# Optimization experiments

Measured on AMD Instinct MI355X. Metric: run time of the kernel, lower is better.

The kernel has to match this reference:

```python
import jax, jax.numpy as jnp
import numpy as np

NUM_HEADS = 16
EMB = 1024
HEAD_DIM = EMB // NUM_HEADS


def setup_inputs() -> dict:
    key = jax.random.key(0)
    ks = jax.random.split(key, 9)
    N, L = 2, 2048
    return {
        "keys": jax.random.normal(ks[0], (N, L, EMB), dtype=jnp.float32),
        "queries": jax.random.normal(ks[1], (N, L, EMB), dtype=jnp.float32),
        "values": jax.random.normal(ks[2], (N, L, EMB), dtype=jnp.float32),
        "mask": jax.random.randint(ks[3], (N, L), 0, 2, dtype=jnp.int32),
        "Wk": jax.random.normal(ks[4], (HEAD_DIM, HEAD_DIM), dtype=jnp.float32) * 0.05,
        "Wq": jax.random.normal(ks[5], (HEAD_DIM, HEAD_DIM), dtype=jnp.float32) * 0.05,
        "Wv": jax.random.normal(ks[6], (HEAD_DIM, HEAD_DIM), dtype=jnp.float32) * 0.05,
        "Wo": jax.random.normal(ks[7], (EMB, EMB), dtype=jnp.float32) * 0.02,
        "bo": jax.random.normal(ks[8], (EMB,), dtype=jnp.float32) * 0.02,
    }


def reference(keys, queries, values, mask, Wk, Wq, Wv, Wo, bo):
    N, Q, E = queries.shape
    H, D = NUM_HEADS, HEAD_DIM
    # reshape to heads: [N, L, H, D]
    k = keys.reshape(N, -1, H, D) @ Wk.T
    q = queries.reshape(N, -1, H, D) @ Wq.T
    # faithful to source bug: values are the v-projection of the projected queries
    v = q @ Wv.T
    # energy: [N, H, Q, K]
    energy = jnp.einsum("nqhd,nkhd->nhqk", q, k)
    m = mask[:, None, None, :]  # [N,1,1,K]
    energy = jnp.where(m == 0, jnp.float32(-1e20), energy)
    p = jax.nn.softmax(energy / jnp.sqrt(jnp.float32(E)), axis=3)
    attn = jnp.einsum("nhqk,nkhd->nqhd", p, v).reshape(N, Q, E)
    return attn @ Wo.T + bo
```

## Files before the change

### kernel.cpp

```cpp
#include <hip/hip_runtime.h>
#include <cmath>

constexpr int N_ = 2;
constexpr int L_ = 2048;
constexpr int H_ = 16;
constexpr int E_ = 1024;
constexpr int ROWS_ = N_ * L_ * H_;

typedef __attribute__((ext_vector_type(8))) short bf16x8;
typedef __attribute__((ext_vector_type(4))) float f32x4;
typedef unsigned short ushort_t;
#define MFMA16(a, b, c) __builtin_amdgcn_mfma_f32_16x16x32_bf16(a, b, c, 0, 0, 0)

__device__ __forceinline__ unsigned short f2bf(float x) {
    union { float f; unsigned u; } v; v.f = x;
    return (unsigned short)((v.u + 0x7fffu + ((v.u >> 16) & 1u)) >> 16);
}
__device__ __forceinline__ unsigned pack2(float a, float b) {
    return (unsigned)f2bf(a) | ((unsigned)f2bf(b) << 16);
}

__global__ __launch_bounds__(256) void proj_kernel(
    const float* __restrict__ keys, const float* __restrict__ queries,
    const float* __restrict__ Wk, const float* __restrict__ Wq, const float* __restrict__ Wv,
    ushort_t* __restrict__ qo, ushort_t* __restrict__ ko, ushort_t* __restrict__ vto)
{
    constexpr int P = 72;
    __shared__ __align__(16) ushort_t Xq[64 * P];
    __shared__ __align__(16) ushort_t Xk[64 * P];
    __shared__ __align__(16) ushort_t Wqs[64 * P];
    __shared__ __align__(16) ushort_t Wks[64 * P];
    __shared__ __align__(16) ushort_t Wvs[64 * P];
    const int tid = threadIdx.x;
    const int lt = blockIdx.x & 31;
    const int h  = (blockIdx.x >> 5) & 15;
    const int n  = blockIdx.x >> 9;
    const int r0 = tid >> 4, c4 = (tid & 15) * 4;

#pragma unroll
    for (int j = 0; j < 4; ++j) {
        const int r = r0 + 16 * j;
        const size_t xoff = (size_t)(n * L_ + lt * 64 + r) * E_ + h * 64 + c4;
        const float4 xq = *(const float4*)&queries[xoff];
        const float4 xk = *(const float4*)&keys[xoff];
        const float4 wq = *(const float4*)&Wq[r * 64 + c4];
        const float4 wk = *(const float4*)&Wk[r * 64 + c4];
        const float4 wv = *(const float4*)&Wv[r * 64 + c4];
        *(uint2*)&Xq[r * P + c4]  = make_uint2(pack2(xq.x, xq.y), pack2(xq.z, xq.w));
        *(uint2*)&Xk[r * P + c4]  = make_uint2(pack2(xk.x, xk.y), pack2(xk.z, xk.w));
        *(uint2*)&Wqs[r * P + c4] = make_uint2(pack2(wq.x, wq.y), pack2(wq.z, wq.w));
        *(uint2*)&Wks[r * P + c4] = make_uint2(pack2(wk.x, wk.y), pack2(wk.z, wk.w));
        *(uint2*)&Wvs[r * P + c4] = make_uint2(pack2(wv.x, wv.y), pack2(wv.z, wv.w));
    }
    __syncthreads();

    const int wave = tid >> 6, lane = tid & 63;
    const int quad = lane >> 4, l16 = lane & 15;
    const int arow = (wave * 16 + l16) * P;
    const f32x4 zero = (f32x4){0.f, 0.f, 0.f, 0.f};

    bf16x8 a0 = *(const bf16x8*)&Xq[arow + quad * 8];
    bf16x8 a1 = *(const bf16x8*)&Xq[arow + 32 + quad * 8];
    bf16x8 c0 = *(const bf16x8*)&Xk[arow + quad * 8];
    bf16x8 c1 = *(const bf16x8*)&Xk[arow + 32 + quad * 8];
    f32x4 qf[4], kf[4];
#pragma unroll
    for (int nt = 0; nt < 4; ++nt) {
        const int brow = (nt * 16 + l16) * P;
        f32x4 acc = MFMA16(a0, *(const bf16x8*)&Wqs[brow + quad * 8], zero);
        qf[nt] = MFMA16(a1, *(const bf16x8*)&Wqs[brow + 32 + quad * 8], acc);
        acc = MFMA16(c0, *(const bf16x8*)&Wks[brow + quad * 8], zero);
        kf[nt] = MFMA16(c1, *(const bf16x8*)&Wks[brow + 32 + quad * 8], acc);
    }
    __syncthreads();

    const int crow = wave * 16 + quad * 4;
#pragma unroll
    for (int nt = 0; nt < 4; ++nt)
#pragma unroll
        for (int reg = 0; reg < 4; ++reg) {
            Xq[(crow + reg) * P + nt * 16 + l16]  = f2bf(qf[nt][reg]);
            Wqs[(crow + reg) * P + nt * 16 + l16] = f2bf(kf[nt][reg]);
        }
    asm volatile("s_waitcnt lgkmcnt(0)" ::: "memory");

    bf16x8 va0 = *(const bf16x8*)&Xq[arow + quad * 8];
    bf16x8 va1 = *(const bf16x8*)&Xq[arow + 32 + quad * 8];
    f32x4 vf[4];
#pragma unroll
    for (int nt = 0; nt < 4; ++nt) {
        const int brow = (nt * 16 + l16) * P;
        f32x4 acc = MFMA16(va0, *(const bf16x8*)&Wvs[brow + quad * 8], zero);
        vf[nt] = MFMA16(va1, *(const bf16x8*)&Wvs[brow + 32 + quad * 8], acc);
    }
#pragma unroll
    for (int nt = 0; nt < 4; ++nt)
#pragma unroll
        for (int reg = 0; reg < 4; ++reg)
            Xk[(nt * 16 + l16) * P + crow + reg] = f2bf(vf[nt][reg]);
    __syncthreads();

#pragma unroll
    for (int j = 0; j < 4; ++j) {
        const int r = r0 + 16 * j;
        const size_t qkoff = (size_t)(n * L_ + lt * 64 + r) * E_ + h * 64 + c4;
        *(uint2*)&qo[qkoff] = *(const uint2*)&Xq[r * P + c4];
        *(uint2*)&ko[qkoff] = *(const uint2*)&Wqs[r * P + c4];
        const size_t vtoff = ((size_t)(n * H_ + h) * 64 + r) * L_ + lt * 64 + c4;
        *(uint2*)&vto[vtoff] = *(const uint2*)&Xk[r * P + c4];
    }
}

__global__ __launch_bounds__(256) void attn_kernel(
    const ushort_t* __restrict__ q, const ushort_t* __restrict__ k,
    const ushort_t* __restrict__ vt, const int* __restrict__ mask,
    ushort_t* __restrict__ attn)
{
    constexpr int P = 72;
    constexpr float CEXP = 0.04508422002778010648f;
    __shared__ __align__(16) ushort_t Qs[64 * P];
    __shared__ __align__(16) ushort_t Ks[64 * P];
    __shared__ __align__(16) ushort_t VTs[64 * P];
    __shared__ __align__(16) ushort_t Ps[64 * P];
    __shared__ float Msk[64];

    const int tid = threadIdx.x;
    const int qt = blockIdx.x & 31;
    const int h  = (blockIdx.x >> 5) & 15;
    const int n  = blockIdx.x >> 9;
    const int r0 = tid >> 4, c4 = (tid & 15) * 4;

#pragma unroll
    for (int j = 0; j < 4; ++j) {
        const int r = r0 + 16 * j;
        *(uint2*)&Qs[r * P + c4] =
            *(const uint2*)&q[(size_t)(n * L_ + qt * 64 + r) * E_ + h * 64 + c4];
    }
    const size_t kbase = (size_t)n * L_ * E_ + h * 64 + c4;
    const size_t vbase = (size_t)(n * H_ + h) * 64 * L_ + c4;
    uint2 kr[4], vr[4];
#pragma unroll
    for (int j = 0; j < 4; ++j) {
        const int r = r0 + 16 * j;
        kr[j] = *(const uint2*)&k[kbase + (size_t)r * E_];
        vr[j] = *(const uint2*)&vt[vbase + (size_t)r * L_];
    }
    int mr = (tid < 64) ? mask[n * L_ + tid] : 0;
    __syncthreads();

    const int wave = tid >> 6, lane = tid & 63;
    const int quad = lane >> 4, l16 = lane & 15;
    const f32x4 zero = (f32x4){0.f, 0.f, 0.f, 0.f};
    const bf16x8 aq0 = *(const bf16x8*)&Qs[(wave * 16 + l16) * P + quad * 8];
    const bf16x8 aq1 = *(const bf16x8*)&Qs[(wave * 16 + l16) * P + 32 + quad * 8];

    float lrow[4] = {0.f, 0.f, 0.f, 0.f};
    f32x4 O[4];
#pragma unroll
    for (int r = 0; r < 4; ++r) O[r] = zero;

    for (int t = 0; t < 32; ++t) {
#pragma unroll
        for (int j = 0; j < 4; ++j) {
            const int r = r0 + 16 * j;
            *(uint2*)&Ks[r * P + c4]  = kr[j];
            *(uint2*)&VTs[r * P + c4] = vr[j];
        }
        if (tid < 64) Msk[tid] = mr ? 0.f : -1e9f;
        __syncthreads();

        const int tt = (t < 31) ? t + 1 : 31;
#pragma unroll
        for (int j = 0; j < 4; ++j) {
            const int r = r0 + 16 * j;
            kr[j] = *(const uint2*)&k[kbase + (size_t)(tt * 64 + r) * E_];
            vr[j] = *(const uint2*)&vt[vbase + (size_t)r * L_ + tt * 64];
        }
        if (tid < 64) mr = mask[n * L_ + tt * 64 + tid];

        f32x4 s[4];
#pragma unroll
        for (int nk = 0; nk < 4; ++nk) {
            const int brow = (nk * 16 + l16) * P;
            f32x4 acc = MFMA16(aq0, *(const bf16x8*)&Ks[brow + quad * 8], zero);
            s[nk] = MFMA16(aq1, *(const bf16x8*)&Ks[brow + 32 + quad * 8], acc);
        }
        float mc[4];
#pragma unroll
        for (int nk = 0; nk < 4; ++nk) mc[nk] = Msk[nk * 16 + l16];

#pragma unroll
        for (int reg = 0; reg < 4; ++reg) {
            const int prow = (wave * 16 + quad * 4 + reg) * P;
            float ls = 0.f;
#pragma unroll
            for (int nk = 0; nk < 4; ++nk) {
                const float e = __builtin_amdgcn_exp2f(fmaf(s[nk][reg], CEXP, mc[nk]));
                ls += e;
                Ps[prow + nk * 16 + l16] = f2bf(e);
            }
            lrow[reg] += ls;
        }
        asm volatile("s_waitcnt lgkmcnt(0)" ::: "memory");

        const bf16x8 ap0 = *(const bf16x8*)&Ps[(wave * 16 + l16) * P + quad * 8];
        const bf16x8 ap1 = *(const bf16x8*)&Ps[(wave * 16 + l16) * P + 32 + quad * 8];
#pragma unroll
        for (int dt = 0; dt < 4; ++dt) {
            const int brow = (dt * 16 + l16) * P;
            O[dt] = MFMA16(ap0, *(const bf16x8*)&VTs[brow + quad * 8], O[dt]);
            O[dt] = MFMA16(ap1, *(const bf16x8*)&VTs[brow + 32 + quad * 8], O[dt]);
        }
        __syncthreads();
    }

#pragma unroll
    for (int reg = 0; reg < 4; ++reg) {
        float s = lrow[reg];
        s += __shfl_xor(s, 1); s += __shfl_xor(s, 2);
        s += __shfl_xor(s, 4); s += __shfl_xor(s, 8);
        lrow[reg] = 1.f / s;
    }
#pragma unroll
    for (int dt = 0; dt < 4; ++dt)
#pragma unroll
        for (int reg = 0; reg < 4; ++reg) {
            const size_t rowg = (size_t)(n * L_ + qt * 64 + wave * 16 + quad * 4 + reg);
            attn[rowg * E_ + h * 64 + dt * 16 + l16] = f2bf(O[dt][reg] * lrow[reg]);
        }
}

__global__ __launch_bounds__(256) void conv_wo_kernel(
    const float* __restrict__ Wo, ushort_t* __restrict__ Wob)
{
    const int i = (blockIdx.x * 256 + threadIdx.x) * 4;
    const float4 w = *(const float4*)&Wo[i];
    *(uint2*)&Wob[i] = make_uint2(pack2(w.x, w.y), pack2(w.z, w.w));
}

__global__ __launch_bounds__(256) void outproj_kernel(
    const ushort_t* __restrict__ attn, const ushort_t* __restrict__ Wob,
    const float* __restrict__ bo, float* __restrict__ out)
{
    constexpr int P = 72;
    __shared__ __align__(16) ushort_t As[64 * P];
    __shared__ __align__(16) ushort_t Bs[128 * P];
    const int tid = threadIdx.x;
    const int bc = (blockIdx.x & 7) * 128;
    const int br = (blockIdx.x >> 3) * 64;
    const int r0 = tid >> 4, c4 = (tid & 15) * 4;
    const int wave = tid >> 6, lane = tid & 63;
    const int quad = lane >> 4, l16 = lane & 15;

    uint2 ar[4], brg[8];
#pragma unroll
    for (int j = 0; j < 4; ++j)
        ar[j] = *(const uint2*)&attn[(size_t)(br + r0 + 16 * j) * E_ + c4];
#pragma unroll
    for (int j = 0; j < 8; ++j)
        brg[j] = *(const uint2*)&Wob[(size_t)(bc + r0 + 16 * j) * E_ + c4];

    f32x4 acc[8];
#pragma unroll
    for (int nt = 0; nt < 8; ++nt) acc[nt] = (f32x4){0.f, 0.f, 0.f, 0.f};

    for (int kt = 0; kt < 16; ++kt) {
#pragma unroll
        for (int j = 0; j < 4; ++j) *(uint2*)&As[(r0 + 16 * j) * P + c4] = ar[j];
#pragma unroll
        for (int j = 0; j < 8; ++j) *(uint2*)&Bs[(r0 + 16 * j) * P + c4] = brg[j];
        __syncthreads();
        const int knext = (kt < 15) ? (kt + 1) * 64 : kt * 64;
#pragma unroll
        for (int j = 0; j < 4; ++j)
            ar[j] = *(const uint2*)&attn[(size_t)(br + r0 + 16 * j) * E_ + knext + c4];
#pragma unroll
        for (int j = 0; j < 8; ++j)
            brg[j] = *(const uint2*)&Wob[(size_t)(bc + r0 + 16 * j) * E_ + knext + c4];

        const bf16x8 a0 = *(const bf16x8*)&As[(wave * 16 + l16) * P + quad * 8];
        const bf16x8 a1 = *(const bf16x8*)&As[(wave * 16 + l16) * P + 32 + quad * 8];
#pragma unroll
        for (int nt = 0; nt < 8; ++nt) {
            const int brow = (nt * 16 + l16) * P;
            acc[nt] = MFMA16(a0, *(const bf16x8*)&Bs[brow + quad * 8], acc[nt]);
            acc[nt] = MFMA16(a1, *(const bf16x8*)&Bs[brow + 32 + quad * 8], acc[nt]);
        }
        __syncthreads();
    }
#pragma unroll
    for (int nt = 0; nt < 8; ++nt) {
        const float b = bo[bc + nt * 16 + l16];
#pragma unroll
        for (int reg = 0; reg < 4; ++reg)
            out[(size_t)(br + wave * 16 + quad * 4 + reg) * E_ + bc + nt * 16 + l16] =
                acc[nt][reg] + b;
    }
}

extern "C" void kernel_launch(void* const* d_in, const int* in_sizes, int n_in,
                              void* d_out, int out_size, void* d_ws, size_t ws_size,
                              hipStream_t stream)
{
    const float* keys    = (const float*)d_in[0];
    const float* queries = (const float*)d_in[1];
    const int*   mask    = (const int*)d_in[3];
    const float* Wk      = (const float*)d_in[4];
    const float* Wq      = (const float*)d_in[5];
    const float* Wv      = (const float*)d_in[6];
    const float* Wo      = (const float*)d_in[7];
    const float* bo      = (const float*)d_in[8];
    float* out = (float*)d_out;

    ushort_t* qbf  = (ushort_t*)d_ws;
    ushort_t* kbf  = qbf + (size_t)ROWS_ * 64;
    ushort_t* vtbf = kbf + (size_t)ROWS_ * 64;
    ushort_t* abf  = vtbf + (size_t)ROWS_ * 64;
    ushort_t* wob  = abf + (size_t)ROWS_ * 64;

    conv_wo_kernel<<<E_ * E_ / 1024, 256, 0, stream>>>(Wo, wob);
    proj_kernel<<<N_ * H_ * (L_ / 64), 256, 0, stream>>>(keys, queries, Wk, Wq, Wv,
                                                         qbf, kbf, vtbf);
    attn_kernel<<<N_ * H_ * (L_ / 64), 256, 0, stream>>>(qbf, kbf, vtbf, mask, abf);
    outproj_kernel<<<(N_ * L_ / 64) * (E_ / 128), 256, 0, stream>>>(abf, wob, bo, out);
}
```

Baseline: 206.7 us.

## Restructure attention into single-wave blocks with register-resident K/V and transposed S

```diff
diff --git a/kernel.cpp b/kernel.cpp
--- a/kernel.cpp
+++ b/kernel.cpp
@@ -111,131 +111,146 @@
     }
 }
 
-__global__ __launch_bounds__(256) void attn_kernel(
+__global__ __launch_bounds__(64, 2) void attn_kernel(
     const ushort_t* __restrict__ q, const ushort_t* __restrict__ k,
-    const ushort_t* __restrict__ vt, const int* __restrict__ mask,
+    const ushort_t* __restrict__ vt, const float* __restrict__ maskf,
     ushort_t* __restrict__ attn)
 {
     constexpr int P = 72;
     constexpr float CEXP = 0.04508422002778010648f;
-    __shared__ __align__(16) ushort_t Qs[64 * P];
-    __shared__ __align__(16) ushort_t Ks[64 * P];
-    __shared__ __align__(16) ushort_t VTs[64 * P];
-    __shared__ __align__(16) ushort_t Ps[64 * P];
-    __shared__ float Msk[64];
-
-    const int tid = threadIdx.x;
-    const int qt = blockIdx.x & 31;
-    const int h  = (blockIdx.x >> 5) & 15;
-    const int n  = blockIdx.x >> 9;
-    const int r0 = tid >> 4, c4 = (tid & 15) * 4;
-
-#pragma unroll
-    for (int j = 0; j < 4; ++j) {
-        const int r = r0 + 16 * j;
-        *(uint2*)&Qs[r * P + c4] =
-            *(const uint2*)&q[(size_t)(n * L_ + qt * 64 + r) * E_ + h * 64 + c4];
-    }
-    const size_t kbase = (size_t)n * L_ * E_ + h * 64 + c4;
-    const size_t vbase = (size_t)(n * H_ + h) * 64 * L_ + c4;
-    uint2 kr[4], vr[4];
-#pragma unroll
-    for (int j = 0; j < 4; ++j) {
-        const int r = r0 + 16 * j;
-        kr[j] = *(const uint2*)&k[kbase + (size_t)r * E_];
-        vr[j] = *(const uint2*)&vt[vbase + (size_t)r * L_];
-    }
-    int mr = (tid < 64) ? mask[n * L_ + tid] : 0;
-    __syncthreads();
-
-    const int wave = tid >> 6, lane = tid & 63;
-    const int quad = lane >> 4, l16 = lane & 15;
-    const f32x4 zero = (f32x4){0.f, 0.f, 0.f, 0.f};
-    const bf16x8 aq0 = *(const bf16x8*)&Qs[(wave * 16 + l16) * P + quad * 8];
-    const bf16x8 aq1 = *(const bf16x8*)&Qs[(wave * 16 + l16) * P + 32 + quad * 8];
-
-    float lrow[4] = {0.f, 0.f, 0.f, 0.f};
-    f32x4 O[4];
-#pragma unroll
-    for (int r = 0; r < 4; ++r) O[r] = zero;
+    __shared__ __align__(16) ushort_t Ps[32 * P];
+    __shared__ __align__(16) float Ls[32];
+
+    const int b = blockIdx.x;
+    const int qt = b & 63;
+    const int h  = (b >> 6) & 15;
+    const int n  = b >> 10;
+    const int lane = threadIdx.x;
+    const int l16 = lane & 15, quad = lane >> 4;
+
+    const ushort_t* kh = k  + (size_t)n * L_ * E_ + h * 64;
+    const ushort_t* vh = vt + (size_t)(n * H_ + h) * 64 * L_;
+    const float*    mh = maskf + n * L_;
+    const size_t qrow0 = (size_t)(n * L_ + qt * 32);
+
+    bf16x8 qb[2][2];
+#pragma unroll
+    for (int s = 0; s < 2; ++s)
+#pragma unroll
+        for (int c = 0; c < 2; ++c)
+            qb[s][c] = *(const bf16x8*)&q[(qrow0 + s * 16 + l16) * E_ + h * 64 + c * 32 + quad * 8];
+
+    bf16x8 kr[4][2]; f32x4 mf[4]; bf16x8 vr[4][2];
+#pragma unroll
+    for (int mk = 0; mk < 4; ++mk) {
+#pragma unroll
+        for (int c = 0; c < 2; ++c)
+            kr[mk][c] = *(const bf16x8*)&kh[(size_t)(mk * 16 + l16) * E_ + c * 32 + quad * 8];
+        mf[mk] = *(const f32x4*)&mh[mk * 16 + quad * 4];
+    }
+#pragma unroll
+    for (int dt = 0; dt < 4; ++dt)
+#pragma unroll
+        for (int c = 0; c < 2; ++c)
+            vr[dt][c] = *(const bf16x8*)&vh[(size_t)(dt * 16 + l16) * L_ + c * 32 + quad * 8];
+
+    float lacc[2] = {0.f, 0.f};
+    f32x4 O[2][4];
+#pragma unroll
+    for (int s = 0; s < 2; ++s)
+#pragma unroll
+        for (int dt = 0; dt < 4; ++dt) O[s][dt] = (f32x4){0.f, 0.f, 0.f, 0.f};
 
     for (int t = 0; t < 32; ++t) {
-#pragma unroll
-        for (int j = 0; j < 4; ++j) {
-            const int r = r0 + 16 * j;
-            *(uint2*)&Ks[r * P + c4]  = kr[j];
-            *(uint2*)&VTs[r * P + c4] = vr[j];
+        f32x4 sA[2][4];
+#pragma unroll
+        for (int s = 0; s < 2; ++s)
+#pragma unroll
+            for (int mk = 0; mk < 4; ++mk) {
+                f32x4 acc = mf[mk];
+                acc = MFMA16(kr[mk][0], qb[s][0], acc);
+                sA[s][mk] = MFMA16(kr[mk][1], qb[s][1], acc);
+            }
+
+        const int tn = (t < 31) ? t + 1 : 31;
+#pragma unroll
+        for (int mk = 0; mk < 4; ++mk) {
+#pragma unroll
+            for (int c = 0; c < 2; ++c)
+                kr[mk][c] = *(const bf16x8*)&kh[(size_t)(tn * 64 + mk * 16 + l16) * E_ + c * 32 + quad * 8];
+            mf[mk] = *(const f32x4*)&mh[tn * 64 + mk * 16 + quad * 4];
         }
-        if (tid < 64) Msk[tid] = mr ? 0.f : -1e9f;
-        __syncthreads();
-
-        const int tt = (t < 31) ? t + 1 : 31;
-#pragma unroll
-        for (int j = 0; j < 4; ++j) {
-            const int r = r0 + 16 * j;
-            kr[j] = *(const uint2*)&k[kbase + (size_t)(tt * 64 + r) * E_];
-            vr[j] = *(const uint2*)&vt[vbase + (size_t)r * L_ + tt * 64];
-        }
-        if (tid < 64) mr = mask[n * L_ + tt * 64 + tid];
-
-        f32x4 s[4];
-#pragma unroll
-        for (int nk = 0; nk < 4; ++nk) {
-            const int brow = (nk * 16 + l16) * P;
-            f32x4 acc = MFMA16(aq0, *(const bf16x8*)&Ks[brow + quad * 8], zero);
-            s[nk] = MFMA16(aq1, *(const bf16x8*)&Ks[brow + 32 + quad * 8], acc);
-        }
-        float mc[4];
-#pragma unroll
-        for (int nk = 0; nk < 4; ++nk) mc[nk] = Msk[nk * 16 + l16];
-
-#pragma unroll
-        for (int reg = 0; reg < 4; ++reg) {
-            const int prow = (wave * 16 + quad * 4 + reg) * P;
-            float ls = 0.f;
-#pragma unroll
-            for (int nk = 0; nk < 4; ++nk) {
-                const float e = __builtin_amdgcn_exp2f(fmaf(s[nk][reg], CEXP, mc[nk]));
-                ls += e;
-                Ps[prow + nk * 16 + l16] = f2bf(e);
-            }
-            lrow[reg] += ls;
-        }
+
+#pragma unroll
+        for (int s = 0; s < 2; ++s)
+#pragma unroll
+            for (int mk = 0; mk < 4; ++mk) {
+                const float p0 = __builtin_amdgcn_exp2f(sA[s][mk][0] * CEXP);
+                const float p1 = __builtin_amdgcn_exp2f(sA[s][mk][1] * CEXP);
+                const float p2 = __builtin_amdgcn_exp2f(sA[s][mk][2] * CEXP);
+                const float p3 = __builtin_amdgcn_exp2f(sA[s][mk][3] * CEXP);
+                lacc[s] += (p0 + p1) + (p2 + p3);
+                *(uint2*)&Ps[(s * 16 + l16) * P + mk * 16 + quad * 4] =
+                    make_uint2(pack2(p0, p1), pack2(p2, p3));
+            }
         asm volatile("s_waitcnt lgkmcnt(0)" ::: "memory");
 
-        const bf16x8 ap0 = *(const bf16x8*)&Ps[(wave * 16 + l16) * P + quad * 8];
-        const bf16x8 ap1 = *(const bf16x8*)&Ps[(wave * 16 + l16) * P + 32 + quad * 8];
-#pragma unroll
-        for (int dt = 0; dt < 4; ++dt) {
-            const int brow = (dt * 16 + l16) * P;
-            O[dt] = MFMA16(ap0, *(const bf16x8*)&VTs[brow + quad * 8], O[dt]);
-            O[dt] = MFMA16(ap1, *(const bf16x8*)&VTs[brow + 32 + quad * 8], O[dt]);
-        }
-        __syncthreads();
-    }
-
-#pragma unroll
-    for (int reg = 0; reg < 4; ++reg) {
-        float s = lrow[reg];
-        s += __shfl_xor(s, 1); s += __shfl_xor(s, 2);
-        s += __shfl_xor(s, 4); s += __shfl_xor(s, 8);
-        lrow[reg] = 1.f / s;
-    }
-#pragma unroll
-    for (int dt = 0; dt < 4; ++dt)
-#pragma unroll
-        for (int reg = 0; reg < 4; ++reg) {
-            const size_t rowg = (size_t)(n * L_ + qt * 64 + wave * 16 + quad * 4 + reg);
-            attn[rowg * E_ + h * 64 + dt * 16 + l16] = f2bf(O[dt][reg] * lrow[reg]);
-        }
-}
-
-__global__ __launch_bounds__(256) void conv_wo_kernel(
-    const float* __restrict__ Wo, ushort_t* __restrict__ Wob)
-{
-    const int i = (blockIdx.x * 256 + threadIdx.x) * 4;
-    const float4 w = *(const float4*)&Wo[i];
-    *(uint2*)&Wob[i] = make_uint2(pack2(w.x, w.y), pack2(w.z, w.w));
+        bf16x8 pa[2][2];
+#pragma unroll
+        for (int s = 0; s < 2; ++s)
+#pragma unroll
+            for (int c = 0; c < 2; ++c)
+                pa[s][c] = *(const bf16x8*)&Ps[(s * 16 + l16) * P + c * 32 + quad * 8];
+#pragma unroll
+        for (int s = 0; s < 2; ++s)
+#pragma unroll
+            for (int dt = 0; dt < 4; ++dt) {
+                O[s][dt] = MFMA16(pa[s][0], vr[dt][0], O[s][dt]);
+                O[s][dt] = MFMA16(pa[s][1], vr[dt][1], O[s][dt]);
+            }
+
+#pragma unroll
+        for (int dt = 0; dt < 4; ++dt)
+#pragma unroll
+            for (int c = 0; c < 2; ++c)
+                vr[dt][c] = *(const bf16x8*)&vh[(size_t)(dt * 16 + l16) * L_ + tn * 64 + c * 32 + quad * 8];
+    }
+
+#pragma unroll
+    for (int s = 0; s < 2; ++s) {
+        float v = lacc[s];
+        v += __shfl_xor(v, 16);
+        v += __shfl_xor(v, 32);
+        if (quad == 0) Ls[s * 16 + l16] = 1.f / v;
+    }
+    asm volatile("s_waitcnt lgkmcnt(0)" ::: "memory");
+    f32x4 linv[2];
+#pragma unroll
+    for (int s = 0; s < 2; ++s) linv[s] = *(const f32x4*)&Ls[s * 16 + quad * 4];
+
+#pragma unroll
+    for (int s = 0; s < 2; ++s)
+#pragma unroll
+        for (int dt = 0; dt < 4; ++dt)
+#pragma unroll
+            for (int reg = 0; reg < 4; ++reg) {
+                const size_t row = qrow0 + s * 16 + quad * 4 + reg;
+                attn[row * E_ + h * 64 + dt * 16 + l16] = f2bf(O[s][dt][reg] * linv[s][reg]);
+            }
+}
+
+__global__ __launch_bounds__(256) void conv_misc_kernel(
+    const float* __restrict__ Wo, const int* __restrict__ mask,
+    ushort_t* __restrict__ Wob, float* __restrict__ maskf)
+{
+    if (blockIdx.x < 1024) {
+        const int i = (blockIdx.x * 256 + threadIdx.x) * 4;
+        const float4 w = *(const float4*)&Wo[i];
+        *(uint2*)&Wob[i] = make_uint2(pack2(w.x, w.y), pack2(w.z, w.w));
+    } else {
+        const int j = (blockIdx.x - 1024) * 256 + threadIdx.x;
+        if (j < N_ * L_) maskf[j] = mask[j] ? 0.f : -1e9f;
+    }
 }
 
 __global__ __launch_bounds__(256) void outproj_kernel(
@@ -243,59 +258,73 @@
     const float* __restrict__ bo, float* __restrict__ out)
 {
     constexpr int P = 72;
-    __shared__ __align__(16) ushort_t As[64 * P];
-    __shared__ __align__(16) ushort_t Bs[128 * P];
+    __shared__ __align__(16) ushort_t As[128 * P];
+    __shared__ __align__(16) ushort_t Bs[64 * P];
     const int tid = threadIdx.x;
-    const int bc = (blockIdx.x & 7) * 128;
-    const int br = (blockIdx.x >> 3) * 64;
+    const int bc = (blockIdx.x & 15) * 64;
+    const int br = (blockIdx.x >> 4) * 128;
     const int r0 = tid >> 4, c4 = (tid & 15) * 4;
     const int wave = tid >> 6, lane = tid & 63;
     const int quad = lane >> 4, l16 = lane & 15;
 
-    uint2 ar[4], brg[8];
+    uint2 ar[8], brg[4];
+#pragma unroll
+    for (int j = 0; j < 8; ++j)
+        ar[j] = *(const uint2*)&attn[(size_t)(br + r0 + 16 * j) * E_ + c4];
 #pragma unroll
     for (int j = 0; j < 4; ++j)
-        ar[j] = *(const uint2*)&attn[(size_t)(br + r0 + 16 * j) * E_ + c4];
-#pragma unroll
-    for (int j = 0; j < 8; ++j)
         brg[j] = *(const uint2*)&Wob[(size_t)(bc + r0 + 16 * j) * E_ + c4];
 
-    f32x4 acc[8];
-#pragma unroll
-    for (int nt = 0; nt < 8; ++nt) acc[nt] = (f32x4){0.f, 0.f, 0.f, 0.f};
+    f32x4 acc[2][4];
+#pragma unroll
+    for (int s = 0; s < 2; ++s)
+#pragma unroll
+        for (int nt = 0; nt < 4; ++nt) acc[s][nt] = (f32x4){0.f, 0.f, 0.f, 0.f};
 
     for (int kt = 0; kt < 16; ++kt) {
 #pragma unroll
-        for (int j = 0; j < 4; ++j) *(uint2*)&As[(r0 + 16 * j) * P + c4] = ar[j];
-#pragma unroll
-        for (int j = 0; j < 8; ++j) *(uint2*)&Bs[(r0 + 16 * j) * P + c4] = brg[j];
+        for (int j = 0; j < 8; ++j) *(uint2*)&As[(r0 + 16 * j) * P + c4] = ar[j];
+#pragma unroll
+        for (int j = 0; j < 4; ++j) *(uint2*)&Bs[(r0 + 16 * j) * P + c4] = brg[j];
         __syncthreads();
-        const int knext = (kt < 15) ? (kt + 1) * 64 : kt * 64;
+        const int knext = ((kt < 15) ? (kt + 1) : kt) * 64;
+#pragma unroll
+        for (int j = 0; j < 8; ++j)
+            ar[j] = *(const uint2*)&attn[(size_t)(br + r0 + 16 * j) * E_ + knext + c4];
 #pragma unroll
         for (int j = 0; j < 4; ++j)
-            ar[j] = *(const uint2*)&attn[(size_t)(br + r0 + 16 * j) * E_ + knext + c4];
-#pragma unroll
-        for (int j = 0; j < 8; ++j)
             brg[j] = *(const uint2*)&Wob[(size_t)(bc + r0 + 16 * j) * E_ + knext + c4];
 
-        const bf16x8 a0 = *(const bf16x8*)&As[(wave * 16 + l16) * P + quad * 8];
-        const bf16x8 a1 = *(const bf16x8*)&As[(wave * 16 + l16) * P + 32 + quad * 8];
-#pragma unroll
-        for (int nt = 0; nt < 8; ++nt) {
-            const int brow = (nt * 16 + l16) * P;
-            acc[nt] = MFMA16(a0, *(const bf16x8*)&Bs[brow + quad * 8], acc[nt]);
-            acc[nt] = MFMA16(a1, *(const bf16x8*)&Bs[brow + 32 + quad * 8], acc[nt]);
+        bf16x8 aw[2][2], bw[4][2];
+#pragma unroll
+        for (int s = 0; s < 2; ++s)
+#pragma unroll
+            for (int c = 0; c < 2; ++c)
+                aw[s][c] = *(const bf16x8*)&As[(wave * 32 + s * 16 + l16) * P + c * 32 + quad * 8];
+#pragma unroll
+        for (int nt = 0; nt < 4; ++nt)
+#pragma unroll
+            for (int c = 0; c < 2; ++c)
+                bw[nt][c] = *(const bf16x8*)&Bs[(nt * 16 + l16) * P + c * 32 + quad * 8];
+#pragma unroll
+        for (int s = 0; s < 2; ++s)
+#pragma unroll
+            for (int nt = 0; nt < 4; ++nt) {
+                acc[s][nt] = MFMA16(aw[s][0], bw[nt][0], acc[s][nt]);
+                acc[s][nt] = MFMA16(aw[s][1], bw[nt][1], acc[s][nt]);
+            }
+        __syncthreads();
+    }
+#pragma unroll
+    for (int s = 0; s < 2; ++s)
+#pragma unroll
+        for (int nt = 0; nt < 4; ++nt) {
+            const float bias = bo[bc + nt * 16 + l16];
+#pragma unroll
+            for (int reg = 0; reg < 4; ++reg)
+                out[(size_t)(br + wave * 32 + s * 16 + quad * 4 + reg) * E_ + bc + nt * 16 + l16] =
+                    acc[s][nt][reg] + bias;
         }
-        __syncthreads();
-    }
-#pragma unroll
-    for (int nt = 0; nt < 8; ++nt) {
-        const float b = bo[bc + nt * 16 + l16];
-#pragma unroll
-        for (int reg = 0; reg < 4; ++reg)
-            out[(size_t)(br + wave * 16 + quad * 4 + reg) * E_ + bc + nt * 16 + l16] =
-                acc[nt][reg] + b;
-    }
 }
 
 extern "C" void kernel_launch(void* const* d_in, const int* in_sizes, int n_in,
@@ -317,10 +346,11 @@
     ushort_t* vtbf = kbf + (size_t)ROWS_ * 64;
     ushort_t* abf  = vtbf + (size_t)ROWS_ * 64;
     ushort_t* wob  = abf + (size_t)ROWS_ * 64;
-
-    conv_wo_kernel<<<E_ * E_ / 1024, 256, 0, stream>>>(Wo, wob);
+    float*    mskf = (float*)(wob + (size_t)E_ * E_);
+
+    conv_misc_kernel<<<1024 + (N_ * L_ + 255) / 256, 256, 0, stream>>>(Wo, mask, wob, mskf);
     proj_kernel<<<N_ * H_ * (L_ / 64), 256, 0, stream>>>(keys, queries, Wk, Wq, Wv,
                                                          qbf, kbf, vtbf);
-    attn_kernel<<<N_ * H_ * (L_ / 64), 256, 0, stream>>>(qbf, kbf, vtbf, mask, abf);
-    outproj_kernel<<<(N_ * L_ / 64) * (E_ / 128), 256, 0, stream>>>(abf, wob, bo, out);
-}
+    attn_kernel<<<N_ * H_ * (L_ / 32), 64, 0, stream>>>(qbf, kbf, vtbf, mskf, abf);
+    outproj_kernel<<<(N_ * L_ / 128) * (E_ / 64), 256, 0, stream>>>(abf, wob, bo, out);
+}
```

Measured after the change: 259.6 us. 25.6% more time.
